# Kernel optimization log

Measured on AMD Instinct MI355X. Metric: run time of the kernel, lower is better.

## Reference

```python
import jax, jax.numpy as jnp
import numpy as np

N = 100000      # nodes
E = 1600000     # edges (avg degree 16)
IN = 128        # in_channels
H = 4           # heads
C = 32          # out_channels per head
NEG_SLOPE = 0.2 # PyG GATConv default


def setup_inputs() -> dict:
    key = jax.random.key(0)
    k = jax.random.split(key, 6)
    x = jax.random.normal(k[0], (N, IN), jnp.float32)
    edge_index = jax.random.randint(k[1], (2, E), 0, N, jnp.int32)
    # Learned params of GATConv: linear weight, per-head attention vectors, bias
    W = jax.random.normal(k[2], (IN, H * C), jnp.float32) / np.sqrt(IN)
    a_src = jax.random.normal(k[3], (H, C), jnp.float32) * 0.1
    a_dst = jax.random.normal(k[4], (H, C), jnp.float32) * 0.1
    bias = jnp.zeros((H * C,), jnp.float32)
    return {"x": x, "edge_index": edge_index, "W": W,
            "a_src": a_src, "a_dst": a_dst, "bias": bias}


def reference(x, edge_index, W, a_src, a_dst, bias):
    n = x.shape[0]
    # Linear transform, per-head view: [N, H, C]
    h = (x @ W).reshape(n, H, C)
    # Node-level attention halves: alpha_i = <h_i, a>  -> [N, H]
    alpha_src = jnp.einsum('nhc,hc->nh', h, a_src)
    alpha_dst = jnp.einsum('nhc,hc->nh', h, a_dst)
    # add_self_loops=True (PyG default)
    loops = jnp.arange(n, dtype=edge_index.dtype)
    src = jnp.concatenate([edge_index[0], loops])  # [E+N]
    dst = jnp.concatenate([edge_index[1], loops])
    # Edge attention logits with LeakyReLU: [E+N, H]
    e = jax.nn.leaky_relu(alpha_src[src] + alpha_dst[dst], NEG_SLOPE)
    # Numerically stable softmax over incoming edges of each destination node
    m = jax.ops.segment_max(e, dst, num_segments=n)          # [N, H]
    e = jnp.exp(e - m[dst])
    denom = jax.ops.segment_sum(e, dst, num_segments=n)      # [N, H]
    att = e / denom[dst]                                     # [E+N, H]
    # Weighted scatter-aggregate of source features: [N, H, C]
    out = jax.ops.segment_sum(att[:, :, None] * h[src], dst, num_segments=n)
    # concat=True: flatten heads, add bias
    return out.reshape(n, H * C) + bias
```

## Files before the change

kernel.cpp:

```cpp
#include <hip/hip_runtime.h>
#include <stdint.h>


#define NBLK 1024
#define BKT 64
#define CAP 2560

typedef __bf16 bf16x8 __attribute__((ext_vector_type(8)));
typedef float f32x4 __attribute__((ext_vector_type(4)));

__device__ __forceinline__ float lrelu(float x) { return x >= 0.f ? x : 0.2f * x; }
__device__ __forceinline__ float blo(unsigned u) { return __uint_as_float(u << 16); }
__device__ __forceinline__ float bhi(unsigned u) { return __uint_as_float(u & 0xffff0000u); }

__global__ __launch_bounds__(256) void k_wprep(const float* __restrict__ W, __bf16* __restrict__ Wt) {
  int idx = blockIdx.x * 256 + threadIdx.x;
  int nn = idx & 127, k = idx >> 7;
  Wt[nn * 128 + k] = (__bf16)W[k * 128 + nn];
}

__global__ __launch_bounds__(256) void k_gemm(const float* __restrict__ x, const __bf16* __restrict__ Wt,
                                              const float* __restrict__ a_src, const float* __restrict__ a_dst,
                                              __bf16* __restrict__ h, float* __restrict__ asrc,
                                              float* __restrict__ adst, int n) {
  __shared__ __align__(16) char Wl[32768];
  __shared__ __align__(16) __bf16 hbuf[4][16 * 128];
  int t = threadIdx.x;
  {
    const float4* s4 = (const float4*)Wt;
    for (int i = t; i < 2048; i += 256) {
      int f = i << 4;
      int nr = f >> 8, c = f & 255;
      *(float4*)(Wl + ((nr << 8) | (c ^ ((nr & 7) << 4)))) = s4[i];
    }
  }
  __syncthreads();
  int wv = t >> 6, lane = t & 63;
  int arow = lane & 15, ag = lane >> 4, c15 = lane & 15;
  float as_t[8], ad_t[8];
#pragma unroll
  for (int tile = 0; tile < 8; ++tile) {
    as_t[tile] = a_src[tile * 16 + c15];
    ad_t[tile] = a_dst[tile * 16 + c15];
  }
  int strip = blockIdx.x * 64 + wv * 16;
  int row = strip + arow;
  float4 fa[8];
  if (row < n) {
    const float4* xr = (const float4*)(x + (size_t)row * 128);
#pragma unroll
    for (int q = 0; q < 4; ++q) {
      fa[2 * q]     = xr[q * 8 + ag * 2];
      fa[2 * q + 1] = xr[q * 8 + ag * 2 + 1];
    }
  } else {
#pragma unroll
    for (int q = 0; q < 8; ++q) fa[q] = make_float4(0.f, 0.f, 0.f, 0.f);
  }
  bf16x8 af[4];
#pragma unroll
  for (int q = 0; q < 4; ++q) {
    af[q][0] = (__bf16)fa[2 * q].x;     af[q][1] = (__bf16)fa[2 * q].y;
    af[q][2] = (__bf16)fa[2 * q].z;     af[q][3] = (__bf16)fa[2 * q].w;
    af[q][4] = (__bf16)fa[2 * q + 1].x; af[q][5] = (__bf16)fa[2 * q + 1].y;
    af[q][6] = (__bf16)fa[2 * q + 1].z; af[q][7] = (__bf16)fa[2 * q + 1].w;
  }
  f32x4 acc[8];
#pragma unroll
  for (int tile = 0; tile < 8; ++tile) acc[tile] = (f32x4){0.f, 0.f, 0.f, 0.f};
#pragma unroll
  for (int q = 0; q < 4; ++q) {
    int gb = (q * 64) + (ag << 4);
#pragma unroll
    for (int tile = 0; tile < 8; ++tile) {
      int nn = tile * 16 + c15;
      bf16x8 bf = *(const bf16x8*)(Wl + ((nn << 8) | (gb ^ ((nn & 7) << 4))));
      acc[tile] = __builtin_amdgcn_mfma_f32_16x16x32_bf16(af[q], bf, acc[tile], 0, 0, 0);
    }
  }
#pragma unroll
  for (int hh = 0; hh < 4; ++hh) {
#pragma unroll
    for (int r = 0; r < 4; ++r) {
      float vps = acc[2 * hh][r] * as_t[2 * hh] + acc[2 * hh + 1][r] * as_t[2 * hh + 1];
      float vpd = acc[2 * hh][r] * ad_t[2 * hh] + acc[2 * hh + 1][r] * ad_t[2 * hh + 1];
#pragma unroll
      for (int m = 1; m < 16; m <<= 1) {
        vps += __shfl_xor(vps, m, 64);
        vpd += __shfl_xor(vpd, m, 64);
      }
      if (c15 == 0) {
        int ro = strip + ag * 4 + r;
        if (ro < n) { asrc[ro * 4 + hh] = vps; adst[ro * 4 + hh] = vpd; }
      }
    }
  }
#pragma unroll
  for (int tile = 0; tile < 8; ++tile) {
#pragma unroll
    for (int r = 0; r < 4; ++r)
      hbuf[wv][(ag * 4 + r) * 128 + tile * 16 + c15] = (__bf16)acc[tile][r];
  }
  int rr = lane >> 2, qq = lane & 3;
  int ro = strip + rr;
  if (ro < n) {
    const float4* src = (const float4*)&hbuf[wv][rr * 128 + qq * 32];
    float4* dst = (float4*)(h + (size_t)ro * 128 + qq * 32);
    dst[0] = src[0];
    dst[1] = src[1];
    dst[2] = src[2];
    dst[3] = src[3];
  }
}


__global__ __launch_bounds__(256) void k_hist(const int* __restrict__ ei, int* __restrict__ cnt2,
                                              int e, int NB, int CE) {
  __shared__ int hist[2048];
  int t = threadIdx.x, blk = blockIdx.x;
  for (int j = t; j < NB; j += 256) hist[j] = 0;
  __syncthreads();
  int i0 = blk * CE, i1 = min(e, i0 + CE);
  for (int i = i0 + t; i < i1; i += 256) atomicAdd(&hist[ei[e + i] >> 6], 1);
  __syncthreads();
  for (int j = t; j < NB; j += 256) cnt2[j * NBLK + blk] = hist[j];
}

__global__ __launch_bounds__(256) void k_scanA(int* __restrict__ cnt2, int* __restrict__ bsums, int m) {
  __shared__ int wsum[4];
  int t = threadIdx.x, i = blockIdx.x * 256 + t;
  int wv = t >> 6, lane = t & 63;
  int v = (i < m) ? cnt2[i] : 0;
  int sc = v;
#pragma unroll
  for (int ofs = 1; ofs < 64; ofs <<= 1) {
    int u = __shfl_up(sc, ofs, 64);
    if (lane >= ofs) sc += u;
  }
  if (lane == 63) wsum[wv] = sc;
  __syncthreads();
  int base = 0;
  for (int w = 0; w < wv; ++w) base += wsum[w];
  if (i < m) cnt2[i] = base + sc - v;
  if (t == 255) bsums[blockIdx.x] = base + sc;
}

__global__ __launch_bounds__(256) void k_scanB(int* __restrict__ bsums, int nbs) {
  __shared__ int wsum[4];
  int t = threadIdx.x, wv = t >> 6, lane = t & 63;
  int carry = 0;
  for (int c = 0; c < nbs; c += 256) {
    int i = c + t;
    int v = (i < nbs) ? bsums[i] : 0;
    int sc = v;
#pragma unroll
    for (int ofs = 1; ofs < 64; ofs <<= 1) {
      int u = __shfl_up(sc, ofs, 64);
      if (lane >= ofs) sc += u;
    }
    if (lane == 63) wsum[wv] = sc;
    __syncthreads();
    int base = carry;
    for (int w = 0; w < wv; ++w) base += wsum[w];
    if (i < nbs) bsums[i] = base + sc - v;
    carry += wsum[0] + wsum[1] + wsum[2] + wsum[3];
    __syncthreads();
  }
}

__global__ __launch_bounds__(256) void k_scanC(int* __restrict__ cnt2, const int* __restrict__ bsums,
                                               int* __restrict__ boffbg, int m, int NB, int e) {
  int i = blockIdx.x * 256 + threadIdx.x;
  if (i < m) {
    int v = cnt2[i] + bsums[i >> 8];
    cnt2[i] = v;
    if ((i & (NBLK - 1)) == 0) boffbg[i / NBLK] = v;
  }
  if (i == 0) boffbg[NB] = e;
}

__global__ __launch_bounds__(256) void k_fill2(const int* __restrict__ ei, const int* __restrict__ cnt2,
                                               unsigned* __restrict__ ebuf, int e, int NB, int CE) {
  __shared__ int cur[2048];
  int t = threadIdx.x, blk = blockIdx.x;
  for (int j = t; j < NB; j += 256) cur[j] = cnt2[j * NBLK + blk];
  __syncthreads();
  int i0 = blk * CE, i1 = min(e, i0 + CE);
  for (int i = i0 + t; i < i1; i += 256) {
    int s = ei[i], d = ei[e + i];
    int pos = atomicAdd(&cur[d >> 6], 1);
    ebuf[pos] = ((unsigned)(d & 63) << 26) | (unsigned)s;
  }
}

__global__ __launch_bounds__(256) void k_agg(const unsigned* __restrict__ ebuf, const int* __restrict__ boffbg,
                                             const float* __restrict__ asrc, const float* __restrict__ adst,
                                             const unsigned* __restrict__ h32, const float* __restrict__ bias,
                                             float* __restrict__ out, int n) {
  __shared__ int sew[CAP];
  __shared__ int lcnt[BKT], loff[BKT + 1], lcur[BKT];
  int b = blockIdx.x, t = threadIdx.x;
  int wv = t >> 6, lane = t & 63;
  int s0 = boffbg[b], s1 = boffbg[b + 1];
  int cnt = s1 - s0;
  int d0 = b * BKT;
  bool sorted = (cnt <= CAP);
  if (t < BKT) lcnt[t] = 0;
  __syncthreads();
  if (sorted) {
    for (int j = t; j < cnt; j += 256) atomicAdd(&lcnt[ebuf[s0 + j] >> 26], 1);
    __syncthreads();
    if (wv == 0) {
      int v = lcnt[lane];
      int sc = v;
#pragma unroll
      for (int o = 1; o < 64; o <<= 1) {
        int u = __shfl_up(sc, o, 64);
        if (lane >= o) sc += u;
      }
      loff[lane + 1] = sc;
      if (lane == 0) loff[0] = 0;
      lcur[lane] = sc - v;
    }
    __syncthreads();
    for (int j = t; j < cnt; j += 256) {
      unsigned u = ebuf[s0 + j];
      int pos = atomicAdd(&lcur[u >> 26], 1);
      sew[pos] = (int)(u & 0x03FFFFFFu);
    }
    __syncthreads();
  }
  int head = lane >> 4;
  float2 bb = ((const float2*)bias)[lane];
  for (int nd = wv; nd < BKT; nd += 4) {
    int d = d0 + nd;
    if (d >= n) break;
    float adh = adst[d * 4 + head];
    float pself = __expf(lrelu(asrc[d * 4 + head] + adh));
    unsigned su = h32[((unsigned)d << 6) + lane];
    float acc0 = pself * blo(su), acc1 = pself * bhi(su), dtot = pself;
    if (sorted) {
      int j = loff[nd], j1 = loff[nd + 1];
      for (; j + 4 <= j1; j += 4) {
        int sA = sew[j], sB = sew[j + 1], sC = sew[j + 2], sD = sew[j + 3];
        unsigned uA = h32[((unsigned)sA << 6) + lane];
        unsigned uB = h32[((unsigned)sB << 6) + lane];
        unsigned uC = h32[((unsigned)sC << 6) + lane];
        unsigned uD = h32[((unsigned)sD << 6) + lane];
        float pA = __expf(lrelu(asrc[sA * 4 + head] + adh));
        float pB = __expf(lrelu(asrc[sB * 4 + head] + adh));
        float pC = __expf(lrelu(asrc[sC * 4 + head] + adh));
        float pD = __expf(lrelu(asrc[sD * 4 + head] + adh));
        dtot += (pA + pB) + (pC + pD);
        acc0 += pA * blo(uA) + pB * blo(uB) + pC * blo(uC) + pD * blo(uD);
        acc1 += pA * bhi(uA) + pB * bhi(uB) + pC * bhi(uC) + pD * bhi(uD);
      }
      for (; j < j1; ++j) {
        int s = sew[j];
        unsigned u = h32[((unsigned)s << 6) + lane];
        float p = __expf(lrelu(asrc[s * 4 + head] + adh));
        dtot += p;
        acc0 += p * blo(u);
        acc1 += p * bhi(u);
      }
    } else {
      for (int j = s0; j < s1; ++j) {
        unsigned u = ebuf[j];
        if ((int)(u >> 26) != nd) continue;
        int s = (int)(u & 0x03FFFFFFu);
        unsigned hu = h32[((unsigned)s << 6) + lane];
        float p = __expf(lrelu(asrc[s * 4 + head] + adh));
        dtot += p;
        acc0 += p * blo(hu);
        acc1 += p * bhi(hu);
      }
    }
    float inv = 1.f / dtot;
    ((float2*)(out + (size_t)d * 128))[lane] = make_float2(acc0 * inv + bb.x, acc1 * inv + bb.y);
  }
}

extern "C" void kernel_launch(void* const* d_in, const int* in_sizes, int n_in,
                              void* d_out, int out_size, void* d_ws, size_t ws_size,
                              hipStream_t stream) {
  const float* x     = (const float*)d_in[0];
  const int*   ei    = (const int*)d_in[1];
  const float* W     = (const float*)d_in[2];
  const float* a_src = (const float*)d_in[3];
  const float* a_dst = (const float*)d_in[4];
  const float* bias  = (const float*)d_in[5];
  float* out = (float*)d_out;

  int n = in_sizes[0] / 128;
  int e = in_sizes[1] / 2;
  int NB = (n + BKT - 1) / BKT;
  int m = NB * NBLK;
  int gridA = (m + 255) / 256;
  int CE = (e + NBLK - 1) / NBLK;

  char* ws = (char*)d_ws;
  size_t ofs = 0;
  auto alloc = [&](size_t bytes) { void* p = ws + ofs; ofs = (ofs + bytes + 15) & ~(size_t)15; return p; };
  __bf16* h      = (__bf16*)alloc((size_t)n * 128 * sizeof(__bf16));
  unsigned* h32  = (unsigned*)h;
  float* asrc    = (float*)alloc((size_t)n * 4 * sizeof(float));
  float* adst    = (float*)alloc((size_t)n * 4 * sizeof(float));
  int* cnt2      = (int*)alloc((size_t)m * sizeof(int));
  int* bsums     = (int*)alloc((size_t)gridA * sizeof(int));
  int* boffbg    = (int*)alloc((size_t)(NB + 1) * sizeof(int));
  unsigned* ebuf = (unsigned*)alloc((size_t)e * sizeof(unsigned));
  __bf16* Wt     = (__bf16*)alloc((size_t)128 * 128 * sizeof(__bf16));

  hipLaunchKernelGGL(k_wprep, dim3(64), dim3(256), 0, stream, W, Wt);
  hipLaunchKernelGGL(k_gemm, dim3((n + 63) / 64), dim3(256), 0, stream,
                     x, Wt, a_src, a_dst, h, asrc, adst, n);
  hipLaunchKernelGGL(k_hist, dim3(NBLK), dim3(256), 0, stream, ei, cnt2, e, NB, CE);
  hipLaunchKernelGGL(k_scanA, dim3(gridA), dim3(256), 0, stream, cnt2, bsums, m);
  hipLaunchKernelGGL(k_scanB, dim3(1), dim3(256), 0, stream, bsums, gridA);
  hipLaunchKernelGGL(k_scanC, dim3(gridA), dim3(256), 0, stream, cnt2, bsums, boffbg, m, NB, e);
  hipLaunchKernelGGL(k_fill2, dim3(NBLK), dim3(256), 0, stream, ei, cnt2, ebuf, e, NB, CE);
  hipLaunchKernelGGL(k_agg, dim3(NB), dim3(256), 0, stream,
                     ebuf, boffbg, asrc, adst, h32, bias, out, n);
}
```

Measured before the change: 199.3 us.

## Precompute per-edge attention weights in LDS during bucket sort, stored as bf16

```diff
diff --git a/kernel.cpp b/kernel.cpp
--- a/kernel.cpp
+++ b/kernel.cpp
@@ -2,9 +2,9 @@
 #include <stdint.h>
 
 
-#define NBLK 1024
+#define NBLK 512
 #define BKT 64
-#define CAP 2560
+#define CAP 1792
 
 typedef __bf16 bf16x8 __attribute__((ext_vector_type(8)));
 typedef float f32x4 __attribute__((ext_vector_type(4)));
@@ -12,6 +12,11 @@
 __device__ __forceinline__ float lrelu(float x) { return x >= 0.f ? x : 0.2f * x; }
 __device__ __forceinline__ float blo(unsigned u) { return __uint_as_float(u << 16); }
 __device__ __forceinline__ float bhi(unsigned u) { return __uint_as_float(u & 0xffff0000u); }
+__device__ __forceinline__ unsigned pk2(float a, float b) {
+  unsigned short ua = __builtin_bit_cast(unsigned short, (__bf16)a);
+  unsigned short ub = __builtin_bit_cast(unsigned short, (__bf16)b);
+  return ((unsigned)ub << 16) | ua;
+}
 
 __global__ __launch_bounds__(256) void k_wprep(const float* __restrict__ W, __bf16* __restrict__ Wt) {
   int idx = blockIdx.x * 256 + threadIdx.x;
@@ -198,6 +203,8 @@
                                              const unsigned* __restrict__ h32, const float* __restrict__ bias,
                                              float* __restrict__ out, int n) {
   __shared__ int sew[CAP];
+  __shared__ __align__(8) uint2 psw[CAP];
+  __shared__ __align__(16) float adstl[BKT * 4];
   __shared__ int lcnt[BKT], loff[BKT + 1], lcur[BKT];
   int b = blockIdx.x, t = threadIdx.x;
   int wv = t >> 6, lane = t & 63;
@@ -205,7 +212,11 @@
   int cnt = s1 - s0;
   int d0 = b * BKT;
   bool sorted = (cnt <= CAP);
-  if (t < BKT) lcnt[t] = 0;
+  if (t < BKT) {
+    lcnt[t] = 0;
+    if (d0 + t < n) ((float4*)adstl)[t] = ((const float4*)adst)[d0 + t];
+    else ((float4*)adstl)[t] = make_float4(0.f, 0.f, 0.f, 0.f);
+  }
   __syncthreads();
   if (sorted) {
     for (int j = t; j < cnt; j += 256) atomicAdd(&lcnt[ebuf[s0 + j] >> 26], 1);
@@ -225,17 +236,26 @@
     __syncthreads();
     for (int j = t; j < cnt; j += 256) {
       unsigned u = ebuf[s0 + j];
-      int pos = atomicAdd(&lcur[u >> 26], 1);
-      sew[pos] = (int)(u & 0x03FFFFFFu);
+      int dl = u >> 26;
+      int s = (int)(u & 0x03FFFFFFu);
+      float4 as = ((const float4*)asrc)[s];
+      float p0 = __expf(lrelu(as.x + adstl[dl * 4 + 0]));
+      float p1 = __expf(lrelu(as.y + adstl[dl * 4 + 1]));
+      float p2 = __expf(lrelu(as.z + adstl[dl * 4 + 2]));
+      float p3 = __expf(lrelu(as.w + adstl[dl * 4 + 3]));
+      int pos = atomicAdd(&lcur[dl], 1);
+      sew[pos] = s;
+      psw[pos] = make_uint2(pk2(p0, p1), pk2(p2, p3));
     }
     __syncthreads();
   }
   int head = lane >> 4;
+  bool hodd = (head & 1), hhi = (head & 2);
   float2 bb = ((const float2*)bias)[lane];
   for (int nd = wv; nd < BKT; nd += 4) {
     int d = d0 + nd;
     if (d >= n) break;
-    float adh = adst[d * 4 + head];
+    float adh = adstl[nd * 4 + head];
     float pself = __expf(lrelu(asrc[d * 4 + head] + adh));
     unsigned su = h32[((unsigned)d << 6) + lane];
     float acc0 = pself * blo(su), acc1 = pself * bhi(su), dtot = pself;
@@ -243,22 +263,27 @@
       int j = loff[nd], j1 = loff[nd + 1];
       for (; j + 4 <= j1; j += 4) {
         int sA = sew[j], sB = sew[j + 1], sC = sew[j + 2], sD = sew[j + 3];
+        uint2 wA = psw[j], wB = psw[j + 1], wC = psw[j + 2], wD = psw[j + 3];
         unsigned uA = h32[((unsigned)sA << 6) + lane];
         unsigned uB = h32[((unsigned)sB << 6) + lane];
         unsigned uC = h32[((unsigned)sC << 6) + lane];
         unsigned uD = h32[((unsigned)sD << 6) + lane];
-        float pA = __expf(lrelu(asrc[sA * 4 + head] + adh));
-        float pB = __expf(lrelu(asrc[sB * 4 + head] + adh));
-        float pC = __expf(lrelu(asrc[sC * 4 + head] + adh));
-        float pD = __expf(lrelu(asrc[sD * 4 + head] + adh));
+        unsigned vA = hhi ? wA.y : wA.x, vB = hhi ? wB.y : wB.x;
+        unsigned vC = hhi ? wC.y : wC.x, vD = hhi ? wD.y : wD.x;
+        float pA = hodd ? bhi(vA) : blo(vA);
+        float pB = hodd ? bhi(vB) : blo(vB);
+        float pC = hodd ? bhi(vC) : blo(vC);
+        float pD = hodd ? bhi(vD) : blo(vD);
         dtot += (pA + pB) + (pC + pD);
         acc0 += pA * blo(uA) + pB * blo(uB) + pC * blo(uC) + pD * blo(uD);
         acc1 += pA * bhi(uA) + pB * bhi(uB) + pC * bhi(uC) + pD * bhi(uD);
       }
       for (; j < j1; ++j) {
         int s = sew[j];
+        uint2 w = psw[j];
         unsigned u = h32[((unsigned)s << 6) + lane];
-        float p = __expf(lrelu(asrc[s * 4 + head] + adh));
+        unsigned v = hhi ? w.y : w.x;
+        float p = hodd ? bhi(v) : blo(v);
         dtot += p;
         acc0 += p * blo(u);
         acc1 += p * bhi(u);
```

Result: no change. 199.5 us (+0.1%).

## Split aggregation into CSR sort kernel and one-wave-per-node gather

Applied to the files above, without the earlier changes.

```diff
diff --git a/kernel.cpp b/kernel.cpp
--- a/kernel.cpp
+++ b/kernel.cpp
@@ -2,9 +2,8 @@
 #include <stdint.h>
 
 
-#define NBLK 1024
+#define NBLK 512
 #define BKT 64
-#define CAP 2560
 
 typedef __bf16 bf16x8 __attribute__((ext_vector_type(8)));
 typedef float f32x4 __attribute__((ext_vector_type(4)));
@@ -168,22 +167,15 @@
   }
 }
 
-__global__ __launch_bounds__(256) void k_scanC(int* __restrict__ cnt2, const int* __restrict__ bsums,
-                                               int* __restrict__ boffbg, int m, int NB, int e) {
-  int i = blockIdx.x * 256 + threadIdx.x;
-  if (i < m) {
-    int v = cnt2[i] + bsums[i >> 8];
-    cnt2[i] = v;
-    if ((i & (NBLK - 1)) == 0) boffbg[i / NBLK] = v;
-  }
-  if (i == 0) boffbg[NB] = e;
-}
-
 __global__ __launch_bounds__(256) void k_fill2(const int* __restrict__ ei, const int* __restrict__ cnt2,
+                                               const int* __restrict__ bsums,
                                                unsigned* __restrict__ ebuf, int e, int NB, int CE) {
   __shared__ int cur[2048];
   int t = threadIdx.x, blk = blockIdx.x;
-  for (int j = t; j < NB; j += 256) cur[j] = cnt2[j * NBLK + blk];
+  for (int j = t; j < NB; j += 256) {
+    int idx = j * NBLK + blk;
+    cur[j] = cnt2[idx] + bsums[idx >> 8];
+  }
   __syncthreads();
   int i0 = blk * CE, i1 = min(e, i0 + CE);
   for (int i = i0 + t; i < i1; i += 256) {
@@ -193,91 +185,96 @@
   }
 }
 
-__global__ __launch_bounds__(256) void k_agg(const unsigned* __restrict__ ebuf, const int* __restrict__ boffbg,
-                                             const float* __restrict__ asrc, const float* __restrict__ adst,
-                                             const unsigned* __restrict__ h32, const float* __restrict__ bias,
-                                             float* __restrict__ out, int n) {
-  __shared__ int sew[CAP];
-  __shared__ int lcnt[BKT], loff[BKT + 1], lcur[BKT];
+__global__ __launch_bounds__(256) void k_sort(const unsigned* __restrict__ ebuf, const int* __restrict__ cnt2,
+                                              const int* __restrict__ bsums,
+                                              int* __restrict__ off, int* __restrict__ adj, int n, int NB, int e) {
+  __shared__ int lcnt[BKT], lcur[BKT];
   int b = blockIdx.x, t = threadIdx.x;
   int wv = t >> 6, lane = t & 63;
-  int s0 = boffbg[b], s1 = boffbg[b + 1];
+  int i0 = b * NBLK;
+  int s0 = cnt2[i0] + bsums[i0 >> 8];
+  int s1 = e;
+  if (b + 1 < NB) { int i1 = (b + 1) * NBLK; s1 = cnt2[i1] + bsums[i1 >> 8]; }
   int cnt = s1 - s0;
   int d0 = b * BKT;
-  bool sorted = (cnt <= CAP);
   if (t < BKT) lcnt[t] = 0;
   __syncthreads();
-  if (sorted) {
-    for (int j = t; j < cnt; j += 256) atomicAdd(&lcnt[ebuf[s0 + j] >> 26], 1);
-    __syncthreads();
-    if (wv == 0) {
-      int v = lcnt[lane];
-      int sc = v;
-#pragma unroll
-      for (int o = 1; o < 64; o <<= 1) {
-        int u = __shfl_up(sc, o, 64);
-        if (lane >= o) sc += u;
-      }
-      loff[lane + 1] = sc;
-      if (lane == 0) loff[0] = 0;
-      lcur[lane] = sc - v;
-    }
-    __syncthreads();
-    for (int j = t; j < cnt; j += 256) {
-      unsigned u = ebuf[s0 + j];
-      int pos = atomicAdd(&lcur[u >> 26], 1);
-      sew[pos] = (int)(u & 0x03FFFFFFu);
-    }
-    __syncthreads();
-  }
+  for (int j = t; j < cnt; j += 256) atomicAdd(&lcnt[ebuf[s0 + j] >> 26], 1);
+  __syncthreads();
+  if (wv == 0) {
+    int v = lcnt[lane];
+    int sc = v;
+#pragma unroll
+    for (int o = 1; o < 64; o <<= 1) {
+      int u = __shfl_up(sc, o, 64);
+      if (lane >= o) sc += u;
+    }
+    lcur[lane] = sc - v;
+    if (d0 + lane < n) off[d0 + lane] = s0 + sc - v;
+  }
+  if (b == 0 && t == 0) off[n] = e;
+  __syncthreads();
+  for (int j = t; j < cnt; j += 256) {
+    unsigned u = ebuf[s0 + j];
+    int pos = atomicAdd(&lcur[u >> 26], 1);
+    adj[s0 + pos] = (int)(u & 0x03FFFFFFu);
+  }
+}
+
+__global__ __launch_bounds__(256) void k_gather(const int* __restrict__ adj, const int* __restrict__ off,
+                                                const float* __restrict__ asrc, const float* __restrict__ adst,
+                                                const unsigned* __restrict__ h32,
+                                                const float* __restrict__ bias, float* __restrict__ out, int n) {
+  int gid = blockIdx.x * 256 + threadIdx.x;
+  int node = gid >> 6, lane = gid & 63;
+  if (node >= n) return;
   int head = lane >> 4;
+  int o = off[node], oe = off[node + 1];
+  float adh = adst[node * 4 + head];
+  float ps = __expf(lrelu(asrc[node * 4 + head] + adh));
+  unsigned su = h32[((unsigned)node << 6) + lane];
+  float acc0 = ps * blo(su), acc1 = ps * bhi(su), dtot = ps;
+  int j = o;
+  for (; j + 8 <= oe; j += 8) {
+    int sv[8];
+    unsigned hu[8];
+    float av[8];
+#pragma unroll
+    for (int k = 0; k < 8; ++k) sv[k] = adj[j + k];
+#pragma unroll
+    for (int k = 0; k < 8; ++k) {
+      hu[k] = h32[((unsigned)sv[k] << 6) + lane];
+      av[k] = asrc[sv[k] * 4 + head];
+    }
+#pragma unroll
+    for (int k = 0; k < 8; ++k) {
+      float p = __expf(lrelu(av[k] + adh));
+      dtot += p;
+      acc0 += p * blo(hu[k]);
+      acc1 += p * bhi(hu[k]);
+    }
+  }
+  for (; j + 2 <= oe; j += 2) {
+    int sA = adj[j], sB = adj[j + 1];
+    unsigned uA = h32[((unsigned)sA << 6) + lane];
+    unsigned uB = h32[((unsigned)sB << 6) + lane];
+    float pA = __expf(lrelu(asrc[sA * 4 + head] + adh));
+    float pB = __expf(lrelu(asrc[sB * 4 + head] + adh));
+    dtot += pA + pB;
+    acc0 += pA * blo(uA) + pB * blo(uB);
+    acc1 += pA * bhi(uA) + pB * bhi(uB);
+  }
+  if (j < oe) {
+    int s = adj[j];
+    unsigned u = h32[((unsigned)s << 6) + lane];
+    float p = __expf(lrelu(asrc[s * 4 + head] + adh));
+    dtot += p;
+    acc0 += p * blo(u);
+    acc1 += p * bhi(u);
+  }
+  float inv = 1.f / dtot;
   float2 bb = ((const float2*)bias)[lane];
-  for (int nd = wv; nd < BKT; nd += 4) {
-    int d = d0 + nd;
-    if (d >= n) break;
-    float adh = adst[d * 4 + head];
-    float pself = __expf(lrelu(asrc[d * 4 + head] + adh));
-    unsigned su = h32[((unsigned)d << 6) + lane];
-    float acc0 = pself * blo(su), acc1 = pself * bhi(su), dtot = pself;
-    if (sorted) {
-      int j = loff[nd], j1 = loff[nd + 1];
-      for (; j + 4 <= j1; j += 4) {
-        int sA = sew[j], sB = sew[j + 1], sC = sew[j + 2], sD = sew[j + 3];
-        unsigned uA = h32[((unsigned)sA << 6) + lane];
-        unsigned uB = h32[((unsigned)sB << 6) + lane];
-        unsigned uC = h32[((unsigned)sC << 6) + lane];
-        unsigned uD = h32[((unsigned)sD << 6) + lane];
-        float pA = __expf(lrelu(asrc[sA * 4 + head] + adh));
-        float pB = __expf(lrelu(asrc[sB * 4 + head] + adh));
-        float pC = __expf(lrelu(asrc[sC * 4 + head] + adh));
-        float pD = __expf(lrelu(asrc[sD * 4 + head] + adh));
-        dtot += (pA + pB) + (pC + pD);
-        acc0 += pA * blo(uA) + pB * blo(uB) + pC * blo(uC) + pD * blo(uD);
-        acc1 += pA * bhi(uA) + pB * bhi(uB) + pC * bhi(uC) + pD * bhi(uD);
-      }
-      for (; j < j1; ++j) {
-        int s = sew[j];
-        unsigned u = h32[((unsigned)s << 6) + lane];
-        float p = __expf(lrelu(asrc[s * 4 + head] + adh));
-        dtot += p;
-        acc0 += p * blo(u);
-        acc1 += p * bhi(u);
-      }
-    } else {
-      for (int j = s0; j < s1; ++j) {
-        unsigned u = ebuf[j];
-        if ((int)(u >> 26) != nd) continue;
-        int s = (int)(u & 0x03FFFFFFu);
-        unsigned hu = h32[((unsigned)s << 6) + lane];
-        float p = __expf(lrelu(asrc[s * 4 + head] + adh));
-        dtot += p;
-        acc0 += p * blo(hu);
-        acc1 += p * bhi(hu);
-      }
-    }
-    float inv = 1.f / dtot;
-    ((float2*)(out + (size_t)d * 128))[lane] = make_float2(acc0 * inv + bb.x, acc1 * inv + bb.y);
-  }
+  ((float2*)(out + (size_t)node * 128))[lane] = make_float2(acc0 * inv + bb.x, acc1 * inv + bb.y);
 }
 
 extern "C" void kernel_launch(void* const* d_in, const int* in_sizes, int n_in,
@@ -305,10 +302,11 @@
   unsigned* h32  = (unsigned*)h;
   float* asrc    = (float*)alloc((size_t)n * 4 * sizeof(float));
   float* adst    = (float*)alloc((size_t)n * 4 * sizeof(float));
+  int* off       = (int*)alloc((size_t)(n + 1) * sizeof(int));
   int* cnt2      = (int*)alloc((size_t)m * sizeof(int));
   int* bsums     = (int*)alloc((size_t)gridA * sizeof(int));
-  int* boffbg    = (int*)alloc((size_t)(NB + 1) * sizeof(int));
   unsigned* ebuf = (unsigned*)alloc((size_t)e * sizeof(unsigned));
+  int* adj       = (int*)alloc((size_t)e * sizeof(int));
   __bf16* Wt     = (__bf16*)alloc((size_t)128 * 128 * sizeof(__bf16));
 
   hipLaunchKernelGGL(k_wprep, dim3(64), dim3(256), 0, stream, W, Wt);
@@ -317,8 +315,8 @@
   hipLaunchKernelGGL(k_hist, dim3(NBLK), dim3(256), 0, stream, ei, cnt2, e, NB, CE);
   hipLaunchKernelGGL(k_scanA, dim3(gridA), dim3(256), 0, stream, cnt2, bsums, m);
   hipLaunchKernelGGL(k_scanB, dim3(1), dim3(256), 0, stream, bsums, gridA);
-  hipLaunchKernelGGL(k_scanC, dim3(gridA), dim3(256), 0, stream, cnt2, bsums, boffbg, m, NB, e);
-  hipLaunchKernelGGL(k_fill2, dim3(NBLK), dim3(256), 0, stream, ei, cnt2, ebuf, e, NB, CE);
-  hipLaunchKernelGGL(k_agg, dim3(NB), dim3(256), 0, stream,
-                     ebuf, boffbg, asrc, adst, h32, bias, out, n);
-}
+  hipLaunchKernelGGL(k_fill2, dim3(NBLK), dim3(256), 0, stream, ei, cnt2, bsums, ebuf, e, NB, CE);
+  hipLaunchKernelGGL(k_sort, dim3(NB), dim3(256), 0, stream, ebuf, cnt2, bsums, off, adj, n, NB, e);
+  hipLaunchKernelGGL(k_gather, dim3((n * 64 + 255) / 256), dim3(256), 0, stream,
+                     adj, off, asrc, adst, h32, bias, out, n);
+}
```

Result: faster. 179.9 us (-9.7%).
